# Optimization experiments

Measured on AMD Instinct MI355X. Metric: run time of the kernel, lower is better.

Reference implementation:

```python
import jax, jax.numpy as jnp
import numpy as np

B, C, T = 8, 512, 1024
H = 8
D = C // H          # head_dim = 64
K = 64              # max_rel_dist
REL = 2 * K + 1     # 129


def setup_inputs() -> dict:
    key = jax.random.key(0)
    ks = jax.random.split(key, 12)
    s = 0.02
    return {
        "x": jax.random.normal(ks[0], (B, C, T), jnp.float32),
        "x_mask": jnp.ones((B, 1, T), jnp.float32),
        "W_q": jax.random.normal(ks[1], (C, C), jnp.float32) * s,
        "b_q": jnp.zeros((C,), jnp.float32),
        "W_k": jax.random.normal(ks[2], (C, C), jnp.float32) * s,
        "b_k": jnp.zeros((C,), jnp.float32),
        "W_v": jax.random.normal(ks[3], (C, C), jnp.float32) * s,
        "b_v": jnp.zeros((C,), jnp.float32),
        "W_o": jax.random.normal(ks[4], (C, C), jnp.float32) * s,
        "b_o": jnp.zeros((C,), jnp.float32),
        "emb_rel_k": jax.random.normal(ks[5], (REL, D), jnp.float32) * 0.01,
        "emb_rel_v": jax.random.normal(ks[6], (REL, D), jnp.float32) * 0.01,
    }


def _conv1x1(x, W, b):
    # Conv1d with kernel_size=1: (B,C,T) x (Cout,Cin) -> (B,Cout,T)
    return jnp.einsum("oc,bct->bot", W, x) + b[None, :, None]


def _shape_heads(x):
    # (B,C,T) -> (B,H,T,D)
    b = x.shape[0]
    return x.reshape(b, H, D, T).transpose(0, 1, 3, 2)


def reference(x, x_mask, W_q, b_q, W_k, b_k, W_v, b_v, W_o, b_o, emb_rel_k, emb_rel_v):
    q = _shape_heads(_conv1x1(x, W_q, b_q))  # (B,H,T,D)
    k = _shape_heads(_conv1x1(x, W_k, b_k))
    v = _shape_heads(_conv1x1(x, W_v, b_v))

    # relative position indices: clamp(j - i, -K, K) + K  -> (T,T)
    pos = jnp.arange(T)
    rel_idx = jnp.clip(pos[None, :] - pos[:, None], -K, K) + K

    # scores: scaled QK^T plus unscaled relative-key term (faithful to source)
    attn = jnp.einsum("bhid,bhjd->bhij", q, k) / (D ** 0.5)
    rel_k_tt = emb_rel_k[rel_idx]            # (T,T,D)
    attn = attn + jnp.einsum("bhid,ijd->bhij", q, rel_k_tt)

    # key mask: positions with x_mask <= 0 get -1e9
    key_mask = (x_mask <= 0).reshape(x.shape[0], 1, 1, T)
    attn = jnp.where(key_mask, -1e9, attn)
    attn = jax.nn.softmax(attn, axis=-1)     # dropout p=0.0 -> identity

    y = jnp.einsum("bhij,bhjd->bhid", attn, v)
    rel_v_tt = emb_rel_v[rel_idx]            # (T,T,D)
    y = y + jnp.einsum("bhij,ijd->bhid", attn, rel_v_tt)

    # (B,H,T,D) -> (B,H,D,T) -> (B,C,T)
    y = y.transpose(0, 1, 3, 2).reshape(x.shape[0], C, T)
    y = _conv1x1(y, W_o, b_o)
    return y * x_mask
```

## Files before the change

### kernel.cpp

```cpp
#include <hip/hip_runtime.h>

#define B_   8
#define C_   512
#define T_   1024
#define H_   8
#define D_   64
#define K_   64
#define REL_ 129

typedef unsigned short u16;
typedef __attribute__((ext_vector_type(8))) short short8;
typedef __attribute__((ext_vector_type(4))) float f32x4;

__device__ __forceinline__ float b2f(u16 u) {
    return __uint_as_float(((unsigned)u) << 16);
}
__device__ __forceinline__ u16 f2b(float f) {
    unsigned x = __float_as_uint(f);
    x += 0x7fffu + ((x >> 16) & 1u);
    return (u16)(x >> 16);
}

__global__ __launch_bounds__(256) void cast_all_kernel(
    const float* __restrict__ x,
    const float* __restrict__ Wq, const float* __restrict__ Wk,
    const float* __restrict__ Wv, const float* __restrict__ Wo,
    const float* __restrict__ erk, const float* __restrict__ erv,
    u16* __restrict__ xt, u16* __restrict__ Wh,
    u16* __restrict__ ervt, u16* __restrict__ erkb)
{
    __shared__ u16 tile[64][72];
    const int blk = blockIdx.x;
    const int tid = threadIdx.x;
    if (blk < 1024) {
        const int t0 = (blk & 15) * 64, c0 = ((blk >> 4) & 7) * 64, b = blk >> 7;
        const int f = tid & 15, r0 = tid >> 4;
#pragma unroll
        for (int p = 0; p < 4; ++p) {
            const int c = r0 + p * 16;
            const float4 v = *(const float4*)(x + ((size_t)b * C_ + c0 + c) * T_ + t0 + f * 4);
            tile[c][f * 4 + 0] = f2b(v.x);
            tile[c][f * 4 + 1] = f2b(v.y);
            tile[c][f * 4 + 2] = f2b(v.z);
            tile[c][f * 4 + 3] = f2b(v.w);
        }
        __syncthreads();
#pragma unroll
        for (int p = 0; p < 4; ++p) {
            const int t = r0 + p * 16;
            ushort4 u;
            u.x = tile[f * 4 + 0][t];
            u.y = tile[f * 4 + 1][t];
            u.z = tile[f * 4 + 2][t];
            u.w = tile[f * 4 + 3][t];
            *(ushort4*)(xt + ((size_t)b * T_ + t0 + t) * C_ + c0 + f * 4) = u;
        }
    } else if (blk < 2048) {
        const int gid = (blk - 1024) * 256 + tid;
        const int s = gid >> 16;
        const int off = (gid & 65535) * 4;
        const float* W = (s == 0) ? Wq : (s == 1) ? Wk : (s == 2) ? Wv : Wo;
        const float4 v = *(const float4*)(W + off);
        ushort4 u;
        u.x = f2b(v.x); u.y = f2b(v.y); u.z = f2b(v.z); u.w = f2b(v.w);
        *(ushort4*)(Wh + ((size_t)s << 18) + off) = u;
    } else {
        const int idx = (blk - 2048) * 256 + tid;
        if (idx < 64 * 160) {
            const int d = idx / 160, rel = idx % 160;
            ervt[idx] = (rel < REL_) ? f2b(erv[rel * D_ + d]) : (u16)0;
        } else {
            const int j = idx - 64 * 160;
            if (j < REL_ * D_) erkb[j] = f2b(erk[j]);
        }
    }
}

__global__ __launch_bounds__(256) void proj_mfma(
    const u16* __restrict__ xt, const u16* __restrict__ Wh,
    const float* __restrict__ bq, const float* __restrict__ bk, const float* __restrict__ bv,
    u16* __restrict__ qh, u16* __restrict__ kh, u16* __restrict__ vt)
{
    __shared__ u16 Wt[64][72];

    const int t0 = blockIdx.x * 64;
    const int h  = blockIdx.y;
    const int sel = blockIdx.z >> 3;
    const int b   = blockIdx.z & 7;
    const int tid = threadIdx.x, wave = tid >> 6, lane = tid & 63;
    const int quad = lane >> 4, l16 = lane & 15;

    const u16* Wbase = Wh + ((size_t)sel << 18) + ((size_t)(h * 64) << 9);
    const u16* A = xt + (((size_t)b * T_ + t0 + wave * 16 + l16) << 9);

    const int so = tid >> 2;
    const int sc = (tid & 3) * 16;
    const u16* wsrc = Wbase + ((size_t)so << 9) + sc;

    f32x4 acc[4] = {{0.f,0.f,0.f,0.f},{0.f,0.f,0.f,0.f},{0.f,0.f,0.f,0.f},{0.f,0.f,0.f,0.f}};

    uint4 wv0 = *(const uint4*)(wsrc);
    uint4 wv1 = *(const uint4*)(wsrc + 8);
#pragma unroll 1
    for (int i = 0; i < 8; ++i) {
        const int c0 = i * 64;
        __syncthreads();
        *(uint4*)&Wt[so][sc] = wv0;
        *(uint4*)&Wt[so][sc + 8] = wv1;
        __syncthreads();
        if (i < 7) {
            wv0 = *(const uint4*)(wsrc + c0 + 64);
            wv1 = *(const uint4*)(wsrc + c0 + 72);
        }
#pragma unroll
        for (int kk = 0; kk < 64; kk += 32) {
            const short8 af = *(const short8*)(A + c0 + kk + quad * 8);
#pragma unroll
            for (int nt = 0; nt < 4; ++nt) {
                const short8 bf = *(const short8*)(&Wt[nt * 16 + l16][kk + quad * 8]);
                acc[nt] = __builtin_amdgcn_mfma_f32_16x16x32_bf16(af, bf, acc[nt], 0, 0, 0);
            }
        }
    }

    const float* bias = (sel == 0) ? bq : (sel == 1) ? bk : bv;
    const int bh = b * 8 + h;
#pragma unroll
    for (int nt = 0; nt < 4; ++nt) {
        const int d = nt * 16 + l16;
        const float bo = bias[h * 64 + d];
#pragma unroll
        for (int rix = 0; rix < 4; ++rix) {
            const int t = t0 + wave * 16 + quad * 4 + rix;
            const u16 val = f2b(acc[nt][rix] + bo);
            if (sel == 2) {
                vt[(((size_t)bh * 64 + d) << 10) + t] = val;
            } else {
                u16* dst = sel ? kh : qh;
                dst[(((size_t)bh * T_ + t) << 6) + d] = val;
            }
        }
    }
}

__global__ __launch_bounds__(512, 2) void attn_kernel(
    const u16* __restrict__ qh, const u16* __restrict__ kh, const u16* __restrict__ vt,
    const u16* __restrict__ erkb, const u16* __restrict__ ervt,
    const float* __restrict__ xmask, u16* __restrict__ yf)
{
    __shared__ u16   Sb[32][1032];
    __shared__ u16   sw[32][168];
    __shared__ float red[8][32][2];
    __shared__ float invrow[32];

    const int gid = blockIdx.x;
    const int x8 = gid & 7, r5 = gid >> 3;
    const int bh = x8 + 8 * (r5 >> 5);
    const int i0 = (r5 & 31) * 32;
    const int b = bh >> 3, h = bh & 7;
    const int tid = threadIdx.x, wave = tid >> 6, lane = tid & 63;
    const int quad = lane >> 4, l16 = lane & 15;

    const float LOG2E = 1.4426950408889634f;
    const float SC    = 0.125f * 1.4426950408889634f;

    short8 qa[2][2];
#pragma unroll
    for (int g = 0; g < 2; ++g) {
        const u16* qrow = qh + (((size_t)bh * T_ + i0 + g * 16 + l16) << 6);
        qa[g][0] = *(const short8*)(qrow + quad * 8);
        qa[g][1] = *(const short8*)(qrow + 32 + quad * 8);
    }

    for (int tile = wave; tile < 9; tile += 8) {
        const int rel = tile * 16 + l16;
        const int rl = rel > 128 ? 128 : rel;
        const u16* ep = erkb + rl * 64 + quad * 8;
        const short8 b0 = *(const short8*)(ep);
        const short8 b1 = *(const short8*)(ep + 32);
#pragma unroll
        for (int g = 0; g < 2; ++g) {
            f32x4 m = {0.f, 0.f, 0.f, 0.f};
            m = __builtin_amdgcn_mfma_f32_16x16x32_bf16(qa[g][0], b0, m, 0, 0, 0);
            m = __builtin_amdgcn_mfma_f32_16x16x32_bf16(qa[g][1], b1, m, 0, 0, 0);
            if (rel < 129) {
#pragma unroll
                for (int rix = 0; rix < 4; ++rix)
                    sw[g * 16 + quad * 4 + rix][rel] = f2b(m[rix] * LOG2E);
            }
        }
    }
    __syncthreads();

    float slo_c[2][4], shi_c[2][4];
#pragma unroll
    for (int g = 0; g < 2; ++g)
#pragma unroll
        for (int rix = 0; rix < 4; ++rix) {
            const int row = g * 16 + quad * 4 + rix;
            slo_c[g][rix] = b2f(sw[row][0]);
            shi_c[g][rix] = b2f(sw[row][2 * K_]);
        }

    float psum[2][4] = {{0.f,0.f,0.f,0.f},{0.f,0.f,0.f,0.f}};
    float phi [2][4] = {{0.f,0.f,0.f,0.f},{0.f,0.f,0.f,0.f}};
    f32x4 og[4][2];
#pragma unroll
    for (int s = 0; s < 4; ++s)
#pragma unroll
        for (int g = 0; g < 2; ++g) og[s][g] = (f32x4){0.f, 0.f, 0.f, 0.f};

    {
        const u16* kb = kh + ((size_t)bh << 16);
        const u16* vbase = vt + ((size_t)bh << 16);
#pragma unroll 1
        for (int c = 0; c < 4; ++c) {
#pragma unroll
            for (int half = 0; half < 2; ++half) {
                const int ct = c * 2 + half;
                const int j0 = wave * 128 + ct * 16;
                const u16* krow = kb + ((size_t)(j0 + l16) << 6);
                const short8 kb0 = *(const short8*)(krow + quad * 8);
                const short8 kb1 = *(const short8*)(krow + 32 + quad * 8);
                const int j = j0 + l16;
                const float xmv = xmask[b * T_ + j];
                const float clampv = (xmv > 0.f) ? 43.280850f : -2.0e9f;
#pragma unroll
                for (int g = 0; g < 2; ++g) {
                    f32x4 acc = {0.f, 0.f, 0.f, 0.f};
                    acc = __builtin_amdgcn_mfma_f32_16x16x32_bf16(qa[g][0], kb0, acc, 0, 0, 0);
                    acc = __builtin_amdgcn_mfma_f32_16x16x32_bf16(qa[g][1], kb1, acc, 0, 0, 0);
                    const int dd = j0 - (i0 + g * 16);
                    const int ibase = i0 + g * 16 + quad * 4;
                    float ee[4];
                    if (dd <= -79) {
#pragma unroll
                        for (int rix = 0; rix < 4; ++rix)
                            ee[rix] = __builtin_amdgcn_exp2f(
                                fminf(fmaf(acc[rix], SC, slo_c[g][rix]), clampv));
                    } else if (dd >= 79) {
#pragma unroll
                        for (int rix = 0; rix < 4; ++rix)
                            ee[rix] = __builtin_amdgcn_exp2f(
                                fminf(fmaf(acc[rix], SC, shi_c[g][rix]), clampv));
                    } else {
                        const int relb = j - ibase + K_;
#pragma unroll
                        for (int rix = 0; rix < 4; ++rix) {
                            int idx = relb - rix;
                            idx = idx < 0 ? 0 : (idx > 2 * K_ ? 2 * K_ : idx);
                            const int row = g * 16 + quad * 4 + rix;
                            const float sr = b2f(sw[row][idx]);
                            ee[rix] = __builtin_amdgcn_exp2f(
                                fminf(fmaf(acc[rix], SC, sr), clampv));
                        }
                    }
                    unsigned p01, p23;
                    asm("v_cvt_pk_bf16_f32 %0, %1, %2" : "=v"(p01) : "v"(ee[0]), "v"(ee[1]));
                    asm("v_cvt_pk_bf16_f32 %0, %1, %2" : "=v"(p23) : "v"(ee[2]), "v"(ee[3]));
                    const int r0 = g * 16 + quad * 4;
                    Sb[r0 + 0][j] = (u16)(p01 & 0xffffu);
                    Sb[r0 + 1][j] = (u16)(p01 >> 16);
                    Sb[r0 + 2][j] = (u16)(p23 & 0xffffu);
                    Sb[r0 + 3][j] = (u16)(p23 >> 16);
                    const float er0 = __uint_as_float(p01 << 16);
                    const float er1 = __uint_as_float(p01 & 0xffff0000u);
                    const float er2 = __uint_as_float(p23 << 16);
                    const float er3 = __uint_as_float(p23 & 0xffff0000u);
                    psum[g][0] += er0; psum[g][1] += er1;
                    psum[g][2] += er2; psum[g][3] += er3;
                    if (dd >= 79) {
                        phi[g][0] += er0; phi[g][1] += er1;
                        phi[g][2] += er2; phi[g][3] += er3;
                    } else if (dd > -79) {
                        phi[g][0] += (j - ibase >= 64) ? er0 : 0.f;
                        phi[g][1] += (j - ibase >= 65) ? er1 : 0.f;
                        phi[g][2] += (j - ibase >= 66) ? er2 : 0.f;
                        phi[g][3] += (j - ibase >= 67) ? er3 : 0.f;
                    }
                }
            }
            const int kc = wave * 128 + c * 32;
            const short8 pb0 = *(const short8*)(&Sb[l16][kc + quad * 8]);
            const short8 pb1 = *(const short8*)(&Sb[16 + l16][kc + quad * 8]);
#pragma unroll
            for (int s = 0; s < 4; ++s) {
                const short8 af = *(const short8*)(vbase + ((size_t)(s * 16 + l16) << 10) + kc + quad * 8);
                og[s][0] = __builtin_amdgcn_mfma_f32_16x16x32_bf16(af, pb0, og[s][0], 0, 0, 0);
                og[s][1] = __builtin_amdgcn_mfma_f32_16x16x32_bf16(af, pb1, og[s][1], 0, 0, 0);
            }
        }
#pragma unroll
        for (int m = 1; m < 16; m <<= 1)
#pragma unroll
            for (int g = 0; g < 2; ++g)
#pragma unroll
                for (int rix = 0; rix < 4; ++rix) {
                    psum[g][rix] += __shfl_xor(psum[g][rix], m);
                    phi[g][rix]  += __shfl_xor(phi[g][rix], m);
                }
        if (l16 == 0)
#pragma unroll
            for (int g = 0; g < 2; ++g)
#pragma unroll
                for (int rix = 0; rix < 4; ++rix) {
                    const int row = g * 16 + quad * 4 + rix;
                    red[wave][row][0] = psum[g][rix];
                    red[wave][row][1] = phi[g][rix];
                }
    }
    __syncthreads();

    {
        const int rr = tid >> 4;
        const int c0 = tid & 15;
        float sumrow = 0.f, phirow = 0.f;
#pragma unroll
        for (int w = 0; w < 8; ++w) {
            sumrow += red[w][rr][0];
            phirow += red[w][rr][1];
        }
        float intsum = 0.f;
        for (int rel = c0; rel < 168; rel += 16) {
            if (rel == 0 || rel == 2 * K_) continue;
            u16 v = 0;
            if (rel < 2 * K_) {
                const int j = i0 + rr + rel - K_;
                if (j >= 0 && j < T_) v = Sb[rr][j];
                intsum += b2f(v);
            }
            sw[rr][rel] = v;
        }
        intsum += __shfl_xor(intsum, 1);
        intsum += __shfl_xor(intsum, 2);
        intsum += __shfl_xor(intsum, 4);
        intsum += __shfl_xor(intsum, 8);
        if (c0 == 0) {
            sw[rr][2 * K_] = f2b(phirow);
            sw[rr][0]      = f2b(sumrow - intsum - phirow);
            invrow[rr]     = 1.0f / sumrow;
        }
    }
    __syncthreads();

    float* fog = (float*)&Sb[0][0];
#pragma unroll
    for (int s = 0; s < 4; ++s)
#pragma unroll
        for (int g = 0; g < 2; ++g)
            *(f32x4*)&fog[wave * 2048 + ((s * 2 + g) * 64 + lane) * 4] = og[s][g];
    __syncthreads();

    {
        const int s = wave >> 1, g = wave & 1;
        const int dh = s * 16 + l16;
        const u16* ep = ervt + dh * 160;
        const int base = ((s * 2 + g) * 64 + lane) * 4;
        const f32x4 a0 = *(const f32x4*)&fog[0 * 2048 + base];
        const f32x4 a1 = *(const f32x4*)&fog[1 * 2048 + base];
        const f32x4 a2 = *(const f32x4*)&fog[2 * 2048 + base];
        const f32x4 a3 = *(const f32x4*)&fog[3 * 2048 + base];
        const f32x4 a4 = *(const f32x4*)&fog[4 * 2048 + base];
        const f32x4 a5 = *(const f32x4*)&fog[5 * 2048 + base];
        const f32x4 a6 = *(const f32x4*)&fog[6 * 2048 + base];
        const f32x4 a7 = *(const f32x4*)&fog[7 * 2048 + base];
        f32x4 accg;
#pragma unroll
        for (int rix = 0; rix < 4; ++rix)
            accg[rix] = ((a0[rix] + a1[rix]) + (a2[rix] + a3[rix]))
                      + ((a4[rix] + a5[rix]) + (a6[rix] + a7[rix]));
#pragma unroll
        for (int kt = 0; kt < 5; ++kt) {
            const short8 af = *(const short8*)(ep + kt * 32 + quad * 8);
            const short8 p  = *(const short8*)(&sw[g * 16 + l16][kt * 32 + quad * 8]);
            accg = __builtin_amdgcn_mfma_f32_16x16x32_bf16(af, p, accg, 0, 0, 0);
        }
        const int dbase = (h << 6) + s * 16 + quad * 4;
        const float iv = invrow[g * 16 + l16];
        ushort4 u;
        u.x = f2b(accg[0] * iv); u.y = f2b(accg[1] * iv);
        u.z = f2b(accg[2] * iv); u.w = f2b(accg[3] * iv);
        *(ushort4*)(yf + (((size_t)b * T_ + i0 + g * 16 + l16) << 9) + dbase) = u;
    }
}

__global__ __launch_bounds__(256) void outproj_mfma(
    const u16* __restrict__ yf, const u16* __restrict__ Woh, const float* __restrict__ bo,
    const float* __restrict__ xmask, float* __restrict__ out)
{
    __shared__ u16 Yt[64][72];

    const int o0 = blockIdx.x * 64;
    const int b  = blockIdx.y >> 4;
    const int t0 = (blockIdx.y & 15) * 64;
    const int tid = threadIdx.x, wave = tid >> 6, lane = tid & 63;
    const int quad = lane >> 4, l16 = lane & 15;

    const u16* A = Woh + ((size_t)(o0 + wave * 16 + l16) << 9);

    const int so = tid >> 2;
    const int sc = (tid & 3) * 16;
    const u16* ysrc = yf + (((size_t)b * T_ + t0 + so) << 9) + sc;

    f32x4 acc[4] = {{0.f,0.f,0.f,0.f},{0.f,0.f,0.f,0.f},{0.f,0.f,0.f,0.f},{0.f,0.f,0.f,0.f}};

    uint4 wv0 = *(const uint4*)(ysrc);
    uint4 wv1 = *(const uint4*)(ysrc + 8);
#pragma unroll 1
    for (int i = 0; i < 8; ++i) {
        const int c0 = i * 64;
        __syncthreads();
        *(uint4*)&Yt[so][sc] = wv0;
        *(uint4*)&Yt[so][sc + 8] = wv1;
        __syncthreads();
        if (i < 7) {
            wv0 = *(const uint4*)(ysrc + c0 + 64);
            wv1 = *(const uint4*)(ysrc + c0 + 72);
        }
#pragma unroll
        for (int kk = 0; kk < 64; kk += 32) {
            const short8 af = *(const short8*)(A + c0 + kk + quad * 8);
#pragma unroll
            for (int nt = 0; nt < 4; ++nt) {
                const short8 bf = *(const short8*)(&Yt[nt * 16 + l16][kk + quad * 8]);
                acc[nt] = __builtin_amdgcn_mfma_f32_16x16x32_bf16(af, bf, acc[nt], 0, 0, 0);
            }
        }
    }

#pragma unroll
    for (int nt = 0; nt < 4; ++nt) {
        const int t = t0 + nt * 16 + l16;
        const float xmv = xmask[b * T_ + t];
#pragma unroll
        for (int rix = 0; rix < 4; ++rix) {
            const int o = o0 + wave * 16 + quad * 4 + rix;
            out[((size_t)b * C_ + o) * T_ + t] = (acc[nt][rix] + bo[o]) * xmv;
        }
    }
}

extern "C" void kernel_launch(void* const* d_in, const int* in_sizes, int n_in,
                              void* d_out, int out_size, void* d_ws, size_t ws_size,
                              hipStream_t stream) {
    const float* x     = (const float*)d_in[0];
    const float* xmask = (const float*)d_in[1];
    const float* Wq    = (const float*)d_in[2];
    const float* bq    = (const float*)d_in[3];
    const float* Wk    = (const float*)d_in[4];
    const float* bk    = (const float*)d_in[5];
    const float* Wv    = (const float*)d_in[6];
    const float* bv    = (const float*)d_in[7];
    const float* Wo    = (const float*)d_in[8];
    const float* bo    = (const float*)d_in[9];
    const float* erk   = (const float*)d_in[10];
    const float* erv   = (const float*)d_in[11];

    const size_t need = 44077184;
    if (ws_size < need) return;
    u16* xt   = (u16*)d_ws;
    u16* Wh   = (u16*)((char*)d_ws + 8388608);
    u16* qh   = (u16*)((char*)d_ws + 10485760);
    u16* kh   = (u16*)((char*)d_ws + 18874368);
    u16* vt   = (u16*)((char*)d_ws + 27262976);
    u16* yf   = (u16*)((char*)d_ws + 35651584);
    u16* ervt = (u16*)((char*)d_ws + 44040192);
    u16* erkb = (u16*)((char*)d_ws + 44060672);
    float* out = (float*)d_out;

    cast_all_kernel<<<dim3(2121), 256, 0, stream>>>(
        x, Wq, Wk, Wv, Wo, erk, erv, xt, Wh, ervt, erkb);
    proj_mfma<<<dim3(T_ / 64, H_, 3 * B_), 256, 0, stream>>>(
        xt, Wh, bq, bk, bv, qh, kh, vt);
    attn_kernel<<<dim3(2048), 512, 0, stream>>>(
        qh, kh, vt, erkb, ervt, xmask, yf);
    outproj_mfma<<<dim3(C_ / 64, B_ * (T_ / 64)), 256, 0, stream>>>(
        yf, Wh + ((size_t)3 << 18), bo, xmask, out);
}
```

Measured before the change: 259.7 us.

## Halve attention block to four waves, each covering 256 keys

The attention kernel now launches 256 threads per block instead of 512. Each wave processes 256 key columns instead of 128, and the cross-wave reductions and final rel-v epilogue are reworked for four waves, with each wave handling both row groups. This halves the cross-wave partial output reduction and sync cost per block, but gives each wave twice the serial work and fewer waves in flight per block. Occupancy depends on LDS usage, which is roughly unchanged per block.

```diff
diff --git a/kernel.cpp b/kernel.cpp
--- a/kernel.cpp
+++ b/kernel.cpp
@@ -143,14 +143,14 @@
     }
 }
 
-__global__ __launch_bounds__(512, 2) void attn_kernel(
+__global__ __launch_bounds__(256, 2) void attn_kernel(
     const u16* __restrict__ qh, const u16* __restrict__ kh, const u16* __restrict__ vt,
     const u16* __restrict__ erkb, const u16* __restrict__ ervt,
     const float* __restrict__ xmask, u16* __restrict__ yf)
 {
     __shared__ u16   Sb[32][1032];
     __shared__ u16   sw[32][168];
-    __shared__ float red[8][32][2];
+    __shared__ float red[4][32][2];
     __shared__ float invrow[32];
 
     const int gid = blockIdx.x;
@@ -172,7 +172,7 @@
         qa[g][1] = *(const short8*)(qrow + 32 + quad * 8);
     }
 
-    for (int tile = wave; tile < 9; tile += 8) {
+    for (int tile = wave; tile < 9; tile += 4) {
         const int rel = tile * 16 + l16;
         const int rl = rel > 128 ? 128 : rel;
         const u16* ep = erkb + rl * 64 + quad * 8;
@@ -214,11 +214,11 @@
         const u16* kb = kh + ((size_t)bh << 16);
         const u16* vbase = vt + ((size_t)bh << 16);
 #pragma unroll 1
-        for (int c = 0; c < 4; ++c) {
+        for (int c = 0; c < 8; ++c) {
 #pragma unroll
             for (int half = 0; half < 2; ++half) {
                 const int ct = c * 2 + half;
-                const int j0 = wave * 128 + ct * 16;
+                const int j0 = wave * 256 + ct * 16;
                 const u16* krow = kb + ((size_t)(j0 + l16) << 6);
                 const short8 kb0 = *(const short8*)(krow + quad * 8);
                 const short8 kb1 = *(const short8*)(krow + 32 + quad * 8);
@@ -280,7 +280,7 @@
                     }
                 }
             }
-            const int kc = wave * 128 + c * 32;
+            const int kc = wave * 256 + c * 32;
             const short8 pb0 = *(const short8*)(&Sb[l16][kc + quad * 8]);
             const short8 pb1 = *(const short8*)(&Sb[16 + l16][kc + quad * 8]);
 #pragma unroll
@@ -312,16 +312,12 @@
     __syncthreads();
 
     {
-        const int rr = tid >> 4;
-        const int c0 = tid & 15;
-        float sumrow = 0.f, phirow = 0.f;
-#pragma unroll
-        for (int w = 0; w < 8; ++w) {
-            sumrow += red[w][rr][0];
-            phirow += red[w][rr][1];
-        }
+        const int rr = tid >> 3;
+        const int c0 = tid & 7;
+        const float sumrow = red[0][rr][0] + red[1][rr][0] + red[2][rr][0] + red[3][rr][0];
+        const float phirow = red[0][rr][1] + red[1][rr][1] + red[2][rr][1] + red[3][rr][1];
         float intsum = 0.f;
-        for (int rel = c0; rel < 168; rel += 16) {
+        for (int rel = c0; rel < 168; rel += 8) {
             if (rel == 0 || rel == 2 * K_) continue;
             u16 v = 0;
             if (rel < 2 * K_) {
@@ -334,7 +330,6 @@
         intsum += __shfl_xor(intsum, 1);
         intsum += __shfl_xor(intsum, 2);
         intsum += __shfl_xor(intsum, 4);
-        intsum += __shfl_xor(intsum, 8);
         if (c0 == 0) {
             sw[rr][2 * K_] = f2b(phirow);
             sw[rr][0]      = f2b(sumrow - intsum - phirow);
@@ -352,35 +347,37 @@
     __syncthreads();
 
     {
-        const int s = wave >> 1, g = wave & 1;
-        const int dh = s * 16 + l16;
+        const int dh = wave * 16 + l16;
         const u16* ep = ervt + dh * 160;
-        const int base = ((s * 2 + g) * 64 + lane) * 4;
-        const f32x4 a0 = *(const f32x4*)&fog[0 * 2048 + base];
-        const f32x4 a1 = *(const f32x4*)&fog[1 * 2048 + base];
-        const f32x4 a2 = *(const f32x4*)&fog[2 * 2048 + base];
-        const f32x4 a3 = *(const f32x4*)&fog[3 * 2048 + base];
-        const f32x4 a4 = *(const f32x4*)&fog[4 * 2048 + base];
-        const f32x4 a5 = *(const f32x4*)&fog[5 * 2048 + base];
-        const f32x4 a6 = *(const f32x4*)&fog[6 * 2048 + base];
-        const f32x4 a7 = *(const f32x4*)&fog[7 * 2048 + base];
-        f32x4 accg;
-#pragma unroll
-        for (int rix = 0; rix < 4; ++rix)
-            accg[rix] = ((a0[rix] + a1[rix]) + (a2[rix] + a3[rix]))
-                      + ((a4[rix] + a5[rix]) + (a6[rix] + a7[rix]));
+        f32x4 accg[2];
+#pragma unroll
+        for (int g = 0; g < 2; ++g) {
+            const int base = ((wave * 2 + g) * 64 + lane) * 4;
+            f32x4 a0 = *(const f32x4*)&fog[base];
+            f32x4 a1 = *(const f32x4*)&fog[2048 + base];
+            f32x4 a2 = *(const f32x4*)&fog[4096 + base];
+            f32x4 a3 = *(const f32x4*)&fog[6144 + base];
+#pragma unroll
+            for (int rix = 0; rix < 4; ++rix)
+                accg[g][rix] = (a0[rix] + a1[rix]) + (a2[rix] + a3[rix]);
+        }
 #pragma unroll
         for (int kt = 0; kt < 5; ++kt) {
             const short8 af = *(const short8*)(ep + kt * 32 + quad * 8);
-            const short8 p  = *(const short8*)(&sw[g * 16 + l16][kt * 32 + quad * 8]);
-            accg = __builtin_amdgcn_mfma_f32_16x16x32_bf16(af, p, accg, 0, 0, 0);
-        }
-        const int dbase = (h << 6) + s * 16 + quad * 4;
-        const float iv = invrow[g * 16 + l16];
-        ushort4 u;
-        u.x = f2b(accg[0] * iv); u.y = f2b(accg[1] * iv);
-        u.z = f2b(accg[2] * iv); u.w = f2b(accg[3] * iv);
-        *(ushort4*)(yf + (((size_t)b * T_ + i0 + g * 16 + l16) << 9) + dbase) = u;
+            const short8 p0 = *(const short8*)(&sw[l16][kt * 32 + quad * 8]);
+            const short8 p1 = *(const short8*)(&sw[16 + l16][kt * 32 + quad * 8]);
+            accg[0] = __builtin_amdgcn_mfma_f32_16x16x32_bf16(af, p0, accg[0], 0, 0, 0);
+            accg[1] = __builtin_amdgcn_mfma_f32_16x16x32_bf16(af, p1, accg[1], 0, 0, 0);
+        }
+        const int dbase = (h << 6) + wave * 16 + quad * 4;
+#pragma unroll
+        for (int g = 0; g < 2; ++g) {
+            const float iv = invrow[g * 16 + l16];
+            ushort4 u;
+            u.x = f2b(accg[g][0] * iv); u.y = f2b(accg[g][1] * iv);
+            u.z = f2b(accg[g][2] * iv); u.w = f2b(accg[g][3] * iv);
+            *(ushort4*)(yf + (((size_t)b * T_ + i0 + g * 16 + l16) << 9) + dbase) = u;
+        }
     }
 }
 
@@ -472,7 +469,7 @@
         x, Wq, Wk, Wv, Wo, erk, erv, xt, Wh, ervt, erkb);
     proj_mfma<<<dim3(T_ / 64, H_, 3 * B_), 256, 0, stream>>>(
         xt, Wh, bq, bk, bv, qh, kh, vt);
-    attn_kernel<<<dim3(2048), 512, 0, stream>>>(
+    attn_kernel<<<dim3(2048), 256, 0, stream>>>(
         qh, kh, vt, erkb, ervt, xmask, yf);
     outproj_mfma<<<dim3(C_ / 64, B_ * (T_ / 64)), 256, 0, stream>>>(
         yf, Wh + ((size_t)3 << 18), bo, xmask, out);
```

After: 239.5 us. 1.08x faster.
